# Kernel tuning notes

Measured on AMD Instinct MI355X. Metric: run time of the kernel, lower is better.

## Reference

```python
import jax, jax.numpy as jnp
import numpy as np

NUM_ITERATIONS = 3


def setup_inputs() -> dict:
    key = jax.random.key(0)
    k1, k2 = jax.random.split(key)
    B, K, R, C, O = 32, 32, 2048, 16, 32
    x = jax.random.normal(k1, (B, R, C), dtype=jnp.float32)
    route_weights = jax.random.normal(k2, (K, R, C, O), dtype=jnp.float32)
    return {"x": x, "route_weights": route_weights}


def reference(x, route_weights):
    # priors: [K, B, R, O] (torch keeps an extra singleton dim at axis 3; we
    # drop it since logits/probs broadcast identically, and re-add at the end)
    priors = jnp.einsum('brc,krco->kbro', x, route_weights)
    logits = jnp.zeros_like(priors)
    outputs = None
    for i in range(NUM_ITERATIONS):
        # custom softmax in source normalizes over dim=2 (route nodes)
        probs = jax.nn.softmax(logits, axis=2)
        # squash=False -> sigmoid logit nonlinearity
        outputs = jax.nn.sigmoid(jnp.sum(probs * priors, axis=2, keepdims=True))  # [K,B,1,O]
        if i != NUM_ITERATIONS - 1:
            delta = jnp.sum(priors * outputs, axis=-1, keepdims=True)  # [K,B,R,1]
            logits = logits + delta  # broadcast over O, matches torch broadcast
    # restore torch output shape [K, B, 1, 1, O]
    return outputs[:, :, :, None, :]
```

## Files before the change

kernel.cpp:

```cpp
#include <hip/hip_runtime.h>


#define KK 32
#define BB 32
#define RR 2048
#define CC 16
#define OO 32

__device__ __forceinline__ float sigmoidf_(float v) {
  return 1.0f / (1.0f + __expf(-v));
}

__global__ void __launch_bounds__(256)
transpose_x(const float* __restrict__ x, float* __restrict__ xT) {
  const int r = blockIdx.x;
  const int t = threadIdx.x;
  const int b = t >> 3;
  const int c = (t & 7) * 2;
  const float2 v = *(const float2*)(x + ((size_t)b * RR + r) * CC + c);
  xT[((size_t)r * CC + c) * BB + b]     = v.x;
  xT[((size_t)r * CC + c + 1) * BB + b] = v.y;
}

__global__ void __launch_bounds__(256)
capsule_priors(const float* __restrict__ xT, const float* __restrict__ w,
               float* __restrict__ P, int k0, int kl_mask, int kl_shift) {
  const int bid = blockIdx.x;
  const int kl  = bid & kl_mask;
  const int rt  = bid >> kl_shift;
  const int t   = threadIdx.x;
  const int lane = t & 63;
  const int wid  = t >> 6;
  const int og = lane & 3;
  const int bg = (lane >> 2) & 3;
  const int rq = lane >> 4;

  const int k = k0 + kl;
  const float* __restrict__ wk = w + (size_t)k * ((size_t)RR * CC * OO);

  #pragma unroll
  for (int qq = 0; qq < 2; ++qq) {
    const int q = wid * 2 + qq;
    const int rl = q * 4 + rq;
    const int r  = rt * 32 + rl;

    const float* xr = xT + ((size_t)r * CC) * BB + bg * 8;
    const float* wr = wk + ((size_t)r * CC) * OO + og * 8;

    float4 acc[8][2];
    #pragma unroll
    for (int bb = 0; bb < 8; ++bb) {
      acc[bb][0] = make_float4(0.f, 0.f, 0.f, 0.f);
      acc[bb][1] = make_float4(0.f, 0.f, 0.f, 0.f);
    }

    #pragma unroll
    for (int c = 0; c < CC; ++c) {
      const float4 xf0 = *(const float4*)(xr + c * BB);
      const float4 xf1 = *(const float4*)(xr + c * BB + 4);
      const float4 wf0 = *(const float4*)(wr + c * OO);
      const float4 wf1 = *(const float4*)(wr + c * OO + 4);
      const float xs[8] = {xf0.x, xf0.y, xf0.z, xf0.w, xf1.x, xf1.y, xf1.z, xf1.w};
      #pragma unroll
      for (int bb = 0; bb < 8; ++bb) {
        const float s = xs[bb];
        acc[bb][0].x = fmaf(s, wf0.x, acc[bb][0].x);
        acc[bb][0].y = fmaf(s, wf0.y, acc[bb][0].y);
        acc[bb][0].z = fmaf(s, wf0.z, acc[bb][0].z);
        acc[bb][0].w = fmaf(s, wf0.w, acc[bb][0].w);
        acc[bb][1].x = fmaf(s, wf1.x, acc[bb][1].x);
        acc[bb][1].y = fmaf(s, wf1.y, acc[bb][1].y);
        acc[bb][1].z = fmaf(s, wf1.z, acc[bb][1].z);
        acc[bb][1].w = fmaf(s, wf1.w, acc[bb][1].w);
      }
    }

    #pragma unroll
    for (int bb = 0; bb < 8; ++bb) {
      const int b = bg * 8 + bb;
      float* Pd = P + (((size_t)kl * BB + b) * RR + r) * OO + og * 8;
      *(float4*)(Pd)     = acc[bb][0];
      *(float4*)(Pd + 4) = acc[bb][1];
    }
  }
}

__global__ void __launch_bounds__(1024, 4)
capsule_route(const float* __restrict__ P, float* __restrict__ out, int k0) {
  __shared__ float swv[512];
  __shared__ float sU[32];
  __shared__ float sM[16];
  __shared__ float sZ[16];

  const int bid  = blockIdx.x;
  const int kl   = bid >> 5;
  const int b    = bid & 31;
  const int t    = threadIdx.x;
  const int o4   = t & 7;
  const int G    = t >> 3;
  const int lane = t & 63;
  const int wid  = t >> 6;

  const float* __restrict__ Pb = P + ((size_t)kl * BB + b) * ((size_t)RR * OO);

  float4 preg[16];
  float4 cs = make_float4(0.f, 0.f, 0.f, 0.f);
  #pragma unroll
  for (int j = 0; j < 16; ++j) {
    preg[j] = *(const float4*)(Pb + (size_t)(j * 128 + G) * OO + (o4 << 2));
    cs.x += preg[j].x; cs.y += preg[j].y; cs.z += preg[j].z; cs.w += preg[j].w;
  }

  #pragma unroll
  for (int m = 8; m <= 32; m <<= 1) {
    cs.x += __shfl_xor(cs.x, m);
    cs.y += __shfl_xor(cs.y, m);
    cs.z += __shfl_xor(cs.z, m);
    cs.w += __shfl_xor(cs.w, m);
  }
  if (lane < 8) *(float4*)&swv[(wid << 5) + (o4 << 2)] = cs;
  __syncthreads();
  if (t < OO) {
    float s = 0.f;
    #pragma unroll
    for (int w2 = 0; w2 < 16; ++w2) s += swv[(w2 << 5) + t];
    sU[t] = sigmoidf_(s * (1.0f / 2048.0f));
  }
  __syncthreads();

  #pragma unroll 1
  for (int pass = 0; pass < 2; ++pass) {
    const float4 v = *(const float4*)&sU[o4 << 2];

    float d[16];
    #pragma unroll
    for (int j = 0; j < 16; ++j) {
      d[j] = preg[j].x * v.x + preg[j].y * v.y + preg[j].z * v.z + preg[j].w * v.w;
    }
    #pragma unroll
    for (int j = 0; j < 16; ++j) {
      d[j] += __shfl_xor(d[j], 1);
      d[j] += __shfl_xor(d[j], 2);
      d[j] += __shfl_xor(d[j], 4);
    }

    float mx = d[0];
    #pragma unroll
    for (int j = 1; j < 16; ++j) mx = fmaxf(mx, d[j]);
    mx = fmaxf(mx, __shfl_xor(mx, 8));
    mx = fmaxf(mx, __shfl_xor(mx, 16));
    mx = fmaxf(mx, __shfl_xor(mx, 32));
    if (lane == 0) sM[wid] = mx;
    __syncthreads();
    float M = sM[0];
    #pragma unroll
    for (int w2 = 1; w2 < 16; ++w2) M = fmaxf(M, sM[w2]);

    float z = 0.f;
    float4 acc = make_float4(0.f, 0.f, 0.f, 0.f);
    #pragma unroll
    for (int j = 0; j < 16; ++j) { d[j] = __expf(d[j] - M); z += d[j]; }
    #pragma unroll
    for (int j = 0; j < 16; ++j) {
      acc.x = fmaf(d[j], preg[j].x, acc.x);
      acc.y = fmaf(d[j], preg[j].y, acc.y);
      acc.z = fmaf(d[j], preg[j].z, acc.z);
      acc.w = fmaf(d[j], preg[j].w, acc.w);
    }
    #pragma unroll
    for (int m = 8; m <= 32; m <<= 1) {
      z     += __shfl_xor(z, m);
      acc.x += __shfl_xor(acc.x, m);
      acc.y += __shfl_xor(acc.y, m);
      acc.z += __shfl_xor(acc.z, m);
      acc.w += __shfl_xor(acc.w, m);
    }
    if (lane < 8) {
      *(float4*)&swv[(wid << 5) + (o4 << 2)] = acc;
      if (o4 == 0) sZ[wid] = z;
    }
    __syncthreads();
    if (t < OO) {
      float zz = 0.f, s = 0.f;
      #pragma unroll
      for (int w2 = 0; w2 < 16; ++w2) { zz += sZ[w2]; s += swv[(w2 << 5) + t]; }
      const float fo = s / zz;
      if (pass == 0) {
        sU[t] += sigmoidf_(fo);
      } else {
        out[((size_t)((k0 + kl) * BB + b)) * OO + t] = sigmoidf_(fo);
      }
    }
    __syncthreads();
  }
}

#define THREADS 1024
#define PLDS_FLOATS (1024 * 32)
#define SWV_OFF PLDS_FLOATS
#define SU_OFF (SWV_OFF + 16 * 32)
#define SM_OFF (SU_OFF + 32)
#define SZ_OFF (SM_OFF + 16)
#define SMEM_FLOATS (SZ_OFF + 16)
#define SMEM_BYTES (SMEM_FLOATS * 4)

__global__ void __launch_bounds__(THREADS, 4)
capsule_fused(const float* __restrict__ x, const float* __restrict__ w,
              float* __restrict__ out) {
  extern __shared__ float smem[];
  float* Plds = smem;
  float* swv  = smem + SWV_OFF;
  float* sU   = smem + SU_OFF;
  float* sM   = smem + SM_OFF;
  float* sZ   = smem + SZ_OFF;

  const int t    = threadIdx.x;
  const int o4   = t & 7;
  const int G    = t >> 3;
  const int lane = t & 63;
  const int wid  = t >> 6;
  const int swz  = ((o4 ^ (G & 7)) << 2);

  const int bid  = blockIdx.x;
  const int xcd  = bid & 7;
  const int slot = bid >> 3;
  const int k    = xcd + 8 * (slot >> 5);
  const int b    = slot & 31;

  const float* __restrict__ xb = x + (size_t)b * (RR * CC);
  const float* __restrict__ wk = w + (size_t)k * ((size_t)RR * CC * OO);

  float4 preg[8];
  float4 cs = make_float4(0.f, 0.f, 0.f, 0.f);

  #pragma unroll
  for (int j = 0; j < 16; ++j) {
    const int r = ((j & 8) ? 1024 : 0) + 8 * G + (j & 7);
    const float* xr = xb + r * CC;
    float xs[16];
    *(float4*)&xs[0]  = *(const float4*)(xr + 0);
    *(float4*)&xs[4]  = *(const float4*)(xr + 4);
    *(float4*)&xs[8]  = *(const float4*)(xr + 8);
    *(float4*)&xs[12] = *(const float4*)(xr + 12);
    const float* wr = wk + (size_t)r * (CC * OO) + (o4 << 2);
    float4 a = make_float4(0.f, 0.f, 0.f, 0.f);
    #pragma unroll
    for (int c = 0; c < CC; ++c) {
      const float4 wv = *(const float4*)(wr + c * OO);
      a.x = fmaf(xs[c], wv.x, a.x);
      a.y = fmaf(xs[c], wv.y, a.y);
      a.z = fmaf(xs[c], wv.z, a.z);
      a.w = fmaf(xs[c], wv.w, a.w);
    }
    if (j < 8) {
      *(float4*)&Plds[((8 * G + (j & 7)) << 5) + swz] = a;
    } else {
      preg[j - 8] = a;
    }
    cs.x += a.x; cs.y += a.y; cs.z += a.z; cs.w += a.w;
  }

  #pragma unroll
  for (int m = 8; m <= 32; m <<= 1) {
    cs.x += __shfl_xor(cs.x, m);
    cs.y += __shfl_xor(cs.y, m);
    cs.z += __shfl_xor(cs.z, m);
    cs.w += __shfl_xor(cs.w, m);
  }
  if (lane < 8) *(float4*)&swv[(wid << 5) + (o4 << 2)] = cs;
  __syncthreads();
  if (t < OO) {
    float s = 0.f;
    #pragma unroll
    for (int w2 = 0; w2 < 16; ++w2) s += swv[(w2 << 5) + t];
    sU[t] = sigmoidf_(s * (1.0f / 2048.0f));
  }
  __syncthreads();

  #pragma unroll 1
  for (int pass = 0; pass < 2; ++pass) {
    const float4 v = *(const float4*)&sU[o4 << 2];
    float d[16];
    #pragma unroll
    for (int j = 0; j < 8; ++j) {
      const float4 p = *(const float4*)&Plds[((8 * G + j) << 5) + swz];
      d[j] = p.x * v.x + p.y * v.y + p.z * v.z + p.w * v.w;
    }
    #pragma unroll
    for (int j = 0; j < 8; ++j) {
      const float4 p = preg[j];
      d[8 + j] = p.x * v.x + p.y * v.y + p.z * v.z + p.w * v.w;
    }
    #pragma unroll
    for (int j = 0; j < 16; ++j) {
      d[j] += __shfl_xor(d[j], 1);
      d[j] += __shfl_xor(d[j], 2);
      d[j] += __shfl_xor(d[j], 4);
    }
    float mx = d[0];
    #pragma unroll
    for (int j = 1; j < 16; ++j) mx = fmaxf(mx, d[j]);
    mx = fmaxf(mx, __shfl_xor(mx, 8));
    mx = fmaxf(mx, __shfl_xor(mx, 16));
    mx = fmaxf(mx, __shfl_xor(mx, 32));
    if (lane == 0) sM[wid] = mx;
    __syncthreads();
    float M = sM[0];
    #pragma unroll
    for (int w2 = 1; w2 < 16; ++w2) M = fmaxf(M, sM[w2]);

    float z = 0.f;
    float4 acc = make_float4(0.f, 0.f, 0.f, 0.f);
    #pragma unroll
    for (int j = 0; j < 16; ++j) { d[j] = __expf(d[j] - M); z += d[j]; }
    #pragma unroll
    for (int j = 0; j < 8; ++j) {
      const float4 p = *(const float4*)&Plds[((8 * G + j) << 5) + swz];
      acc.x = fmaf(d[j], p.x, acc.x);
      acc.y = fmaf(d[j], p.y, acc.y);
      acc.z = fmaf(d[j], p.z, acc.z);
      acc.w = fmaf(d[j], p.w, acc.w);
    }
    #pragma unroll
    for (int j = 0; j < 8; ++j) {
      const float4 p = preg[j];
      acc.x = fmaf(d[8 + j], p.x, acc.x);
      acc.y = fmaf(d[8 + j], p.y, acc.y);
      acc.z = fmaf(d[8 + j], p.z, acc.z);
      acc.w = fmaf(d[8 + j], p.w, acc.w);
    }
    #pragma unroll
    for (int m = 8; m <= 32; m <<= 1) {
      z     += __shfl_xor(z, m);
      acc.x += __shfl_xor(acc.x, m);
      acc.y += __shfl_xor(acc.y, m);
      acc.z += __shfl_xor(acc.z, m);
      acc.w += __shfl_xor(acc.w, m);
    }
    if (lane < 8) {
      *(float4*)&swv[(wid << 5) + (o4 << 2)] = acc;
      if (o4 == 0) sZ[wid] = z;
    }
    __syncthreads();
    if (t < OO) {
      float zz = 0.f, s = 0.f;
      #pragma unroll
      for (int w2 = 0; w2 < 16; ++w2) { zz += sZ[w2]; s += swv[(w2 << 5) + t]; }
      const float fo = s / zz;
      if (pass == 0) {
        sU[t] = sU[t] + sigmoidf_(fo);
      } else {
        out[((k << 5) + b) * OO + t] = sigmoidf_(fo);
      }
    }
    __syncthreads();
  }
}

extern "C" void kernel_launch(void* const* d_in, const int* in_sizes, int n_in,
                              void* d_out, int out_size, void* d_ws, size_t ws_size,
                              hipStream_t stream) {
  const float* x = (const float*)d_in[0];
  const float* w = (const float*)d_in[1];
  float* out = (float*)d_out;
  (void)in_sizes; (void)n_in; (void)out_size;

  const size_t perK = (size_t)BB * RR * OO * sizeof(float);
  const size_t xTsz = (size_t)BB * RR * CC * sizeof(float);
  int KCHUNK = 0, SHIFT = 0;
  if      (ws_size >= 16 * perK + xTsz) { KCHUNK = 16; SHIFT = 4; }
  else if (ws_size >=  8 * perK + xTsz) { KCHUNK = 8;  SHIFT = 3; }
  else if (ws_size >=  4 * perK + xTsz) { KCHUNK = 4;  SHIFT = 2; }

  if (KCHUNK == 0) {
    hipFuncSetAttribute(reinterpret_cast<const void*>(capsule_fused),
                        hipFuncAttributeMaxDynamicSharedMemorySize, SMEM_BYTES);
    capsule_fused<<<dim3(KK * BB), dim3(THREADS), SMEM_BYTES, stream>>>(x, w, out);
    return;
  }

  float* P  = (float*)d_ws;
  float* xT = (float*)((char*)d_ws + KCHUNK * perK);

  transpose_x<<<dim3(RR), dim3(256), 0, stream>>>(x, xT);
  for (int k0 = 0; k0 < KK; k0 += KCHUNK) {
    capsule_priors<<<dim3(KCHUNK * 64), dim3(256), 0, stream>>>(
        xT, w, P, k0, KCHUNK - 1, SHIFT);
    capsule_route<<<dim3(KCHUNK * 32), dim3(1024), 0, stream>>>(P, out, k0);
  }
}
```

Before: 221.2 us.

## Shrink per-thread priors tile and cap K-chunk size at eight

The priors kernel is rewritten so each thread computes a 4x8 output tile for one route node instead of an 8x8 tile for two route nodes. This cuts registers per thread and launches 4x more blocks, with a launch bound of 5 blocks per SM, to raise occupancy and hide latency. The K-chunk choice drops the 16 option, so the workspace holds at most 8 K slices. That keeps the priors buffer smaller and more cache-friendly, but doubles the number of priors/route launch pairs. The x loads are reused across fewer outputs, which adds some redundant load traffic.

After: 817.4 us. +269.6%, slower.

```diff
diff --git a/kernel.cpp b/kernel.cpp
--- a/kernel.cpp
+++ b/kernel.cpp
@@ -22,66 +22,58 @@
   xT[((size_t)r * CC + c + 1) * BB + b] = v.y;
 }
 
-__global__ void __launch_bounds__(256)
-capsule_priors(const float* __restrict__ xT, const float* __restrict__ w,
-               float* __restrict__ P, int k0, int kl_mask, int kl_shift) {
-  const int bid = blockIdx.x;
-  const int kl  = bid & kl_mask;
-  const int rt  = bid >> kl_shift;
-  const int t   = threadIdx.x;
+__global__ void __launch_bounds__(256, 5)
+capsule_priors2(const float* __restrict__ xT, const float* __restrict__ w,
+                float* __restrict__ P, int k0) {
+  const int bid  = blockIdx.x;
+  const int kl   = bid >> 8;
+  const int rt   = bid & 255;
+  const int t    = threadIdx.x;
   const int lane = t & 63;
   const int wid  = t >> 6;
-  const int og = lane & 3;
-  const int bg = (lane >> 2) & 3;
-  const int rq = lane >> 4;
-
-  const int k = k0 + kl;
-  const float* __restrict__ wk = w + (size_t)k * ((size_t)RR * CC * OO);
-
-  #pragma unroll
-  for (int qq = 0; qq < 2; ++qq) {
-    const int q = wid * 2 + qq;
-    const int rl = q * 4 + rq;
-    const int r  = rt * 32 + rl;
-
-    const float* xr = xT + ((size_t)r * CC) * BB + bg * 8;
-    const float* wr = wk + ((size_t)r * CC) * OO + og * 8;
-
-    float4 acc[8][2];
-    #pragma unroll
-    for (int bb = 0; bb < 8; ++bb) {
-      acc[bb][0] = make_float4(0.f, 0.f, 0.f, 0.f);
-      acc[bb][1] = make_float4(0.f, 0.f, 0.f, 0.f);
-    }
-
-    #pragma unroll
-    for (int c = 0; c < CC; ++c) {
-      const float4 xf0 = *(const float4*)(xr + c * BB);
-      const float4 xf1 = *(const float4*)(xr + c * BB + 4);
-      const float4 wf0 = *(const float4*)(wr + c * OO);
-      const float4 wf1 = *(const float4*)(wr + c * OO + 4);
-      const float xs[8] = {xf0.x, xf0.y, xf0.z, xf0.w, xf1.x, xf1.y, xf1.z, xf1.w};
-      #pragma unroll
-      for (int bb = 0; bb < 8; ++bb) {
-        const float s = xs[bb];
-        acc[bb][0].x = fmaf(s, wf0.x, acc[bb][0].x);
-        acc[bb][0].y = fmaf(s, wf0.y, acc[bb][0].y);
-        acc[bb][0].z = fmaf(s, wf0.z, acc[bb][0].z);
-        acc[bb][0].w = fmaf(s, wf0.w, acc[bb][0].w);
-        acc[bb][1].x = fmaf(s, wf1.x, acc[bb][1].x);
-        acc[bb][1].y = fmaf(s, wf1.y, acc[bb][1].y);
-        acc[bb][1].z = fmaf(s, wf1.z, acc[bb][1].z);
-        acc[bb][1].w = fmaf(s, wf1.w, acc[bb][1].w);
-      }
-    }
-
-    #pragma unroll
-    for (int bb = 0; bb < 8; ++bb) {
-      const int b = bg * 8 + bb;
-      float* Pd = P + (((size_t)kl * BB + b) * RR + r) * OO + og * 8;
-      *(float4*)(Pd)     = acc[bb][0];
-      *(float4*)(Pd + 4) = acc[bb][1];
-    }
+  const int og   = lane & 3;
+  const int bq   = (lane >> 2) & 7;
+  const int rw   = lane >> 5;
+  const int r    = rt * 8 + wid * 2 + rw;
+  const int k    = k0 + kl;
+
+  const float* __restrict__ xr = xT + ((size_t)r * CC) * BB + bq * 4;
+  const float* __restrict__ wr = w + (size_t)k * ((size_t)RR * CC * OO)
+                                   + ((size_t)r * CC) * OO + og * 8;
+
+  float4 a[4][2];
+  #pragma unroll
+  for (int bb = 0; bb < 4; ++bb) {
+    a[bb][0] = make_float4(0.f, 0.f, 0.f, 0.f);
+    a[bb][1] = make_float4(0.f, 0.f, 0.f, 0.f);
+  }
+
+  #pragma unroll
+  for (int c = 0; c < CC; ++c) {
+    const float4 xf = *(const float4*)(xr + c * BB);
+    const float4 w0 = *(const float4*)(wr + c * OO);
+    const float4 w1 = *(const float4*)(wr + c * OO + 4);
+    const float xs[4] = {xf.x, xf.y, xf.z, xf.w};
+    #pragma unroll
+    for (int bb = 0; bb < 4; ++bb) {
+      const float s = xs[bb];
+      a[bb][0].x = fmaf(s, w0.x, a[bb][0].x);
+      a[bb][0].y = fmaf(s, w0.y, a[bb][0].y);
+      a[bb][0].z = fmaf(s, w0.z, a[bb][0].z);
+      a[bb][0].w = fmaf(s, w0.w, a[bb][0].w);
+      a[bb][1].x = fmaf(s, w1.x, a[bb][1].x);
+      a[bb][1].y = fmaf(s, w1.y, a[bb][1].y);
+      a[bb][1].z = fmaf(s, w1.z, a[bb][1].z);
+      a[bb][1].w = fmaf(s, w1.w, a[bb][1].w);
+    }
+  }
+
+  #pragma unroll
+  for (int bb = 0; bb < 4; ++bb) {
+    const int b = bq * 4 + bb;
+    float* Pd = P + (((size_t)kl * BB + b) * RR + r) * OO + og * 8;
+    *(float4*)(Pd)     = a[bb][0];
+    *(float4*)(Pd + 4) = a[bb][1];
   }
 }
 
@@ -367,10 +359,9 @@
 
   const size_t perK = (size_t)BB * RR * OO * sizeof(float);
   const size_t xTsz = (size_t)BB * RR * CC * sizeof(float);
-  int KCHUNK = 0, SHIFT = 0;
-  if      (ws_size >= 16 * perK + xTsz) { KCHUNK = 16; SHIFT = 4; }
-  else if (ws_size >=  8 * perK + xTsz) { KCHUNK = 8;  SHIFT = 3; }
-  else if (ws_size >=  4 * perK + xTsz) { KCHUNK = 4;  SHIFT = 2; }
+  int KCHUNK = 0;
+  if      (ws_size >= 8 * perK + xTsz) KCHUNK = 8;
+  else if (ws_size >= 4 * perK + xTsz) KCHUNK = 4;
 
   if (KCHUNK == 0) {
     hipFuncSetAttribute(reinterpret_cast<const void*>(capsule_fused),
@@ -384,8 +375,7 @@
 
   transpose_x<<<dim3(RR), dim3(256), 0, stream>>>(x, xT);
   for (int k0 = 0; k0 < KK; k0 += KCHUNK) {
-    capsule_priors<<<dim3(KCHUNK * 64), dim3(256), 0, stream>>>(
-        xT, w, P, k0, KCHUNK - 1, SHIFT);
+    capsule_priors2<<<dim3(KCHUNK * 256), dim3(256), 0, stream>>>(xT, w, P, k0);
     capsule_route<<<dim3(KCHUNK * 32), dim3(1024), 0, stream>>>(P, out, k0);
   }
 }
```
